# Optimization experiments

Measured on AMD Instinct MI355X. Metric: run time of the kernel, lower is better.

Reference implementation:

```python
import jax, jax.numpy as jnp
import numpy as np

N = 50000
E = 1600000

def setup_inputs() -> dict:
    key = jax.random.key(0)
    ks = jax.random.split(key, 8)
    x = jax.random.normal(ks[0], (N, 512), dtype=jnp.float32)
    edge_index = jax.random.randint(ks[1], (2, E), 0, N, dtype=jnp.int32).astype(jnp.int64)
    eigenvectors = jax.random.normal(ks[2], (N, 128), dtype=jnp.float32)
    W1 = jax.random.normal(ks[3], (512, 128), dtype=jnp.float32) * 0.04
    b1 = jnp.zeros((128,), dtype=jnp.float32)
    W2 = jax.random.normal(ks[4], (128, 64), dtype=jnp.float32) * 0.09
    b2 = jnp.zeros((64,), dtype=jnp.float32)
    lin_W = jax.random.normal(ks[5], (128, 64), dtype=jnp.float32) * 0.09
    W3 = jax.random.normal(ks[6], (128, 40), dtype=jnp.float32) * 0.09
    b3 = jnp.zeros((40,), dtype=jnp.float32)
    return {"x": x, "edge_index": edge_index, "eigenvectors": eigenvectors,
            "W1": W1, "b1": b1, "W2": W2, "b2": b2, "lin_W": lin_W, "W3": W3, "b3": b3}

def _gcn_norm(edge_index, num_nodes):
    # add self loops, then symmetric normalization D^-1/2 (A+I) D^-1/2
    loop = jnp.arange(num_nodes, dtype=edge_index.dtype)
    row = jnp.concatenate([edge_index[0], loop])  # source
    col = jnp.concatenate([edge_index[1], loop])  # target
    w = jnp.ones(row.shape[0], dtype=jnp.float32)
    deg = jax.ops.segment_sum(w, col, num_segments=num_nodes)
    dis = jnp.where(deg > 0, 1.0 / jnp.sqrt(deg), 0.0)
    norm = dis[row] * dis[col]  # [E+N]
    return row, col, norm

def _gcn_conv(h, W, b, row, col, norm, num_nodes):
    h = h @ W                                  # [N, d_out] linear first (PyG order)
    msg = h[row] * norm[:, None]               # gather + scale, [E+N, d_out]
    out = jax.ops.segment_sum(msg, col, num_segments=num_nodes)  # scatter-add
    return out + b

def reference(x, edge_index, eigenvectors, W1, b1, W2, b2, lin_W, W3, b3):
    num_nodes = x.shape[0]
    row, col, norm = _gcn_norm(edge_index, num_nodes)
    h = jax.nn.relu(_gcn_conv(x, W1, b1, row, col, norm, num_nodes))
    # dropout omitted: eval mode (deterministic reference)
    h = jax.nn.relu(_gcn_conv(h, W2, b2, row, col, norm, num_nodes))
    xp = eigenvectors @ lin_W                  # Linear(spec_in, spec_out, bias=False)
    h = jnp.concatenate([h, xp], axis=1)       # [N, h2+spec_out]
    h = _gcn_conv(h, W3, b3, row, col, norm, num_nodes)
    return jax.nn.log_softmax(h, axis=1)
```

## Files before the change

### kernel.cpp

```cpp
#include <hip/hip_runtime.h>
#include <cstdint>
#include <cstddef>

constexpr int BLK = 256;
constexpr int NB = 128;

static inline size_t ws_align(size_t x) { return (x + 255) & ~size_t(255); }

typedef __attribute__((ext_vector_type(8))) short bf16x8;
typedef __attribute__((ext_vector_type(4))) float f32x4;

__device__ inline unsigned short f2bf(float f) {
  unsigned int u = __float_as_uint(f);
  unsigned int r = (u + 0x7fffu + ((u >> 16) & 1u)) >> 16;
  return (unsigned short)r;
}
__device__ inline float bf2f(unsigned short u) {
  return __uint_as_float(((unsigned int)u) << 16);
}
__device__ inline float bf2f_lo(unsigned int w) {
  return __uint_as_float(w << 16);
}
__device__ inline float bf2f_hi(unsigned int w) {
  return __uint_as_float(w & 0xffff0000u);
}

__device__ inline void gload16(const void* gp, void* lp) {
  __builtin_amdgcn_global_load_lds(
      (const __attribute__((address_space(1))) void*)gp,
      (__attribute__((address_space(3))) void*)lp, 16, 0, 0);
}

__global__ void k_pack_wt(const int* __restrict__ ei, unsigned int* __restrict__ pk,
                          int* __restrict__ cnt, int E, int nChunk,
                          const float* __restrict__ W1, const float* __restrict__ W2,
                          const float* __restrict__ linW, const float* __restrict__ W3,
                          unsigned short* __restrict__ WT1, unsigned short* __restrict__ WT2,
                          unsigned short* __restrict__ WTl, unsigned short* __restrict__ WT3) {
  if (blockIdx.x >= NB) {
    int i = (blockIdx.x - NB) * BLK + threadIdx.x;
    if (i < 65536) {
      int n = i >> 9, k = i & 511;
      WT1[i] = f2bf(W1[(size_t)k * 128 + n]);
    } else if (i < 73728) {
      int j = i - 65536; int n = j >> 7, k = j & 127;
      WT2[j] = f2bf(W2[(size_t)k * 64 + n]);
    } else if (i < 81920) {
      int j = i - 73728; int n = j >> 7, k = j & 127;
      WTl[j] = f2bf(linW[(size_t)k * 64 + n]);
    } else if (i < 88064) {
      int j = i - 81920; int n = j >> 7, k = j & 127;
      WT3[j] = f2bf(n < 40 ? W3[(size_t)k * 40 + n] : 0.f);
    }
    return;
  }
  __shared__ int hist[256];
  for (int t = threadIdx.x; t < 256; t += BLK) hist[t] = 0;
  __syncthreads();
  int allz = 1;
  #pragma unroll 8
  for (int i = 0; i < 32; ++i) allz &= (ei[2 * i + 1] == 0) ? 1 : 0;
  const bool i64 = allz != 0;
  int beg = blockIdx.x * nChunk, end = min(beg + nChunk, E);
  for (int i = beg + threadIdx.x; i < end; i += BLK) {
    int row, col;
    if (i64) { row = ei[2 * i]; col = ei[2 * (E + i)]; }
    else     { row = ei[i];     col = ei[E + i]; }
    unsigned int p = ((unsigned int)col << 16) | (unsigned int)row;
    pk[i] = p;
    atomicAdd(&hist[col >> 8], 1);
  }
  __syncthreads();
  for (int t = threadIdx.x; t < 256; t += BLK) cnt[blockIdx.x * 256 + t] = hist[t];
}

__global__ void k_wscan(const int* __restrict__ cnt, int* __restrict__ woffs,
                        int* __restrict__ base, int nb, int E) {
  __shared__ int wsums[5];
  int w = threadIdx.x;
  int s = 0;
  for (int b = 0; b < nb; ++b) s += cnt[b * 256 + w];
  int lane = w & 63, wv = w >> 6;
  int x = s;
  #pragma unroll
  for (int sh = 1; sh < 64; sh <<= 1) { int t = __shfl_up(x, sh); if (lane >= sh) x += t; }
  if (lane == 63) wsums[wv] = x;
  __syncthreads();
  if (w == 0) { int a = 0; for (int k = 0; k < 4; ++k) { int t = wsums[k]; wsums[k] = a; a += t; } }
  __syncthreads();
  int excl = x - s + wsums[wv];
  woffs[w] = excl;
  if (w == 255) woffs[256] = excl + s;
  int start = excl;
  for (int b = 0; b < nb; ++b) { base[b * 256 + w] = start; start += cnt[b * 256 + w]; }
}

__global__ __launch_bounds__(256)
void k_part_gemm1(const unsigned int* __restrict__ pk, const int* __restrict__ base,
                  unsigned int* __restrict__ P, int E, int nChunk,
                  const float* __restrict__ x, const unsigned short* __restrict__ WT,
                  unsigned short* __restrict__ C, int N) {
  __shared__ __align__(16) char smem[49152];
  if (blockIdx.x < NB) {
    int* cur = (int*)smem;
    for (int t = threadIdx.x; t < 256; t += BLK) cur[t] = base[blockIdx.x * 256 + t];
    __syncthreads();
    int beg = blockIdx.x * nChunk, end = min(beg + nChunk, E);
    for (int i = beg + threadIdx.x; i < end; i += BLK) {
      unsigned int p = pk[i];
      int pos = atomicAdd(&cur[p >> 24], 1);
      P[pos] = p;
    }
    return;
  }
  float* As0 = (float*)smem;
  unsigned short* Wsl0 = (unsigned short*)(smem + 32768);
  const int tid = threadIdx.x;
  const int lane = tid & 63, wv = tid >> 6;
  const int m = lane & 15, kq = lane >> 4;
  const int row0 = ((int)blockIdx.x - NB) * 128;

  const int r8 = lane >> 3;
  const int c8 = lane & 7;
  int agrow[4];
  #pragma unroll
  for (int jj = 0; jj < 4; ++jj) {
    int gr = row0 + wv * 32 + jj * 8 + r8;
    agrow[jj] = gr < N ? gr : N - 1;
  }

  f32x4 acc[2][8];
  #pragma unroll
  for (int mr = 0; mr < 2; ++mr)
    #pragma unroll
    for (int t = 0; t < 8; ++t) acc[mr][t] = {0.f, 0.f, 0.f, 0.f};

  auto STAGE = [&](int pb, int kb) {
    #pragma unroll
    for (int jj = 0; jj < 4; ++jj) {
      const float* src = x + (size_t)agrow[jj] * 512 + kb * 32 + (c8 ^ r8) * 4;
      gload16(src, As0 + pb * 4096 + (wv * 32 + jj * 8) * 32);
    }
    #pragma unroll
    for (int jj = 0; jj < 2; ++jj) {
      int issue = wv * 2 + jj;
      int slot = issue >> 1, half = issue & 1;
      const unsigned short* src = WT + (size_t)(half * 64 + lane) * 512 + kb * 32 + slot * 8;
      gload16(src, Wsl0 + pb * 4096 + slot * 1024 + half * 512);
    }
  };

  STAGE(0, 0);
  __syncthreads();

  #pragma unroll 1
  for (int t = 0; t < 16; ++t) {
    const int p = t & 1;
    if (t < 15) STAGE(p ^ 1, t + 1);

    const char* Ab = (const char*)(As0 + p * 4096);
    const char* Wb = (const char*)(Wsl0 + p * 4096);
    bf16x8 af[2];
    #pragma unroll
    for (int mr = 0; mr < 2; ++mr) {
      int row = wv * 32 + mr * 16 + m;
      int s = row & 7;
      f32x4 lo = *(const f32x4*)(Ab + row * 128 + ((kq * 2) ^ s) * 16);
      f32x4 hi = *(const f32x4*)(Ab + row * 128 + ((kq * 2 + 1) ^ s) * 16);
      af[mr][0] = (short)f2bf(lo[0]); af[mr][1] = (short)f2bf(lo[1]);
      af[mr][2] = (short)f2bf(lo[2]); af[mr][3] = (short)f2bf(lo[3]);
      af[mr][4] = (short)f2bf(hi[0]); af[mr][5] = (short)f2bf(hi[1]);
      af[mr][6] = (short)f2bf(hi[2]); af[mr][7] = (short)f2bf(hi[3]);
    }
    #pragma unroll
    for (int tt = 0; tt < 8; ++tt) {
      bf16x8 bf = *(const bf16x8*)(Wb + kq * 2048 + (tt * 16 + m) * 16);
      #pragma unroll
      for (int mr = 0; mr < 2; ++mr)
        acc[mr][tt] = __builtin_amdgcn_mfma_f32_16x16x32_bf16(af[mr], bf, acc[mr][tt], 0, 0, 0);
    }
    __syncthreads();
  }

  #pragma unroll
  for (int mr = 0; mr < 2; ++mr)
    #pragma unroll
    for (int r = 0; r < 4; ++r) {
      int rr = row0 + wv * 32 + mr * 16 + kq * 4 + r;
      if (rr < N) {
        #pragma unroll
        for (int t = 0; t < 8; ++t)
          C[(size_t)rr * 128 + t * 16 + m] = f2bf(acc[mr][t][r]);
      }
    }
}

__global__ void k_window_build(const unsigned int* __restrict__ P,
                               const int* __restrict__ woffs,
                               float* __restrict__ dis, int* __restrict__ offs,
                               int* __restrict__ csr, int N, int E) {
  __shared__ int hist[256];
  __shared__ int wsums[5];
  __shared__ int lbase[256];
  const int node0 = blockIdx.x * 256;
  const int t = threadIdx.x;
  hist[t] = 0;
  __syncthreads();
  const int beg = woffs[blockIdx.x], end = woffs[blockIdx.x + 1];
  for (int i = beg + t; i < end; i += BLK)
    atomicAdd(&hist[(P[i] >> 16) & 255], 1);
  __syncthreads();
  const int dg = hist[t];
  if (node0 + t < N) dis[node0 + t] = 1.0f / sqrtf((float)(dg + 1));
  int lane = t & 63, wv = t >> 6;
  int x = dg;
  #pragma unroll
  for (int sh = 1; sh < 64; sh <<= 1) { int q = __shfl_up(x, sh); if (lane >= sh) x += q; }
  if (lane == 63) wsums[wv] = x;
  __syncthreads();
  if (t == 0) { int a = 0; for (int k = 0; k < 4; ++k) { int q = wsums[k]; wsums[k] = a; a += q; } }
  __syncthreads();
  const int goff = beg + (x - dg + wsums[wv]);
  if (node0 + t < N) offs[node0 + t] = goff;
  lbase[t] = goff;
  __syncthreads();
  for (int i = beg + t; i < end; i += BLK) {
    unsigned int p = P[i];
    int pos = atomicAdd(&lbase[(p >> 16) & 255], 1);
    csr[pos] = (int)(p & 0xffffu);
  }
  if (blockIdx.x == 0 && t == 0) offs[N] = E;
}

template<int NT, int MR, bool AF32>
__device__ inline void mgemm_body(int bi, const void* __restrict__ Av,
                                  const unsigned short* __restrict__ WT,
                                  const float* __restrict__ dis, unsigned short* __restrict__ C,
                                  int ldc, int NOUT, int N) {
  constexpr int K = 128;
  const int tid = threadIdx.x;
  const int lane = tid & 63;
  const int wv = tid >> 6;
  const int m = lane & 15;
  const int kq = lane >> 4;
  const int orow = bi * (64 * MR) + wv * (16 * MR);

  int rowc[MR];
  #pragma unroll
  for (int mr = 0; mr < MR; ++mr) {
    int row = orow + mr * 16 + m;
    rowc[mr] = row < N ? row : N - 1;
  }

  f32x4 acc[MR][NT];
  #pragma unroll
  for (int mr = 0; mr < MR; ++mr)
    #pragma unroll
    for (int t = 0; t < NT; ++t) acc[mr][t] = {0.f, 0.f, 0.f, 0.f};

  #pragma unroll 4
  for (int k0 = 0; k0 < K; k0 += 32) {
    bf16x8 af[MR];
    #pragma unroll
    for (int mr = 0; mr < MR; ++mr) {
      if constexpr (AF32) {
        const float* Arow = (const float*)Av + (size_t)rowc[mr] * K + kq * 8 + k0;
        float4 a0 = *(const float4*)Arow;
        float4 a1 = *(const float4*)(Arow + 4);
        af[mr][0] = (short)f2bf(a0.x); af[mr][1] = (short)f2bf(a0.y);
        af[mr][2] = (short)f2bf(a0.z); af[mr][3] = (short)f2bf(a0.w);
        af[mr][4] = (short)f2bf(a1.x); af[mr][5] = (short)f2bf(a1.y);
        af[mr][6] = (short)f2bf(a1.z); af[mr][7] = (short)f2bf(a1.w);
      } else {
        const unsigned short* Arow = (const unsigned short*)Av + (size_t)rowc[mr] * K + kq * 8 + k0;
        af[mr] = *(const bf16x8*)Arow;
      }
    }
    bf16x8 bf[NT];
    #pragma unroll
    for (int t = 0; t < NT; ++t)
      bf[t] = *(const bf16x8*)(WT + (size_t)(t * 16 + m) * K + k0 + kq * 8);
    #pragma unroll
    for (int t = 0; t < NT; ++t)
      #pragma unroll
      for (int mr = 0; mr < MR; ++mr)
        acc[mr][t] = __builtin_amdgcn_mfma_f32_16x16x32_bf16(af[mr], bf[t], acc[mr][t], 0, 0, 0);
  }
  #pragma unroll
  for (int mr = 0; mr < MR; ++mr) {
    #pragma unroll
    for (int r = 0; r < 4; ++r) {
      int rr = orow + mr * 16 + kq * 4 + r;
      if (rr < N) {
        float s = dis ? dis[rr] : 1.f;
        #pragma unroll
        for (int t = 0; t < NT; ++t) {
          int cc = t * 16 + m;
          if (cc < NOUT)
            C[(size_t)rr * ldc + cc] = f2bf(acc[mr][t][r] * s);
        }
      }
    }
  }
}

__global__ __launch_bounds__(256)
void k_mgemm2x(const unsigned short* __restrict__ G, const unsigned short* __restrict__ WT2,
               const float* __restrict__ dis, unsigned short* __restrict__ F,
               const float* __restrict__ eig, const unsigned short* __restrict__ WTl,
               unsigned short* __restrict__ XP, int N, int nA) {
  if ((int)blockIdx.x < nA)
    mgemm_body<4, 2, false>(blockIdx.x, G, WT2, dis, F, 64, 64, N);
  else
    mgemm_body<4, 2, true>(blockIdx.x - nA, eig, WTl, nullptr, XP, 64, 64, N);
}

__global__ __launch_bounds__(256)
void k_mgemm3(const unsigned short* __restrict__ H2, const unsigned short* __restrict__ XP,
              const unsigned short* __restrict__ WT3, const float* __restrict__ dis,
              unsigned short* __restrict__ C, int N) {
  constexpr int NT = 3, MR = 2;
  const int tid = threadIdx.x;
  const int lane = tid & 63;
  const int wv = tid >> 6;
  const int m = lane & 15;
  const int kq = lane >> 4;
  const int orow = blockIdx.x * (64 * MR) + wv * (16 * MR);

  int rowc[MR];
  #pragma unroll
  for (int mr = 0; mr < MR; ++mr) {
    int row = orow + mr * 16 + m;
    rowc[mr] = row < N ? row : N - 1;
  }

  f32x4 acc[MR][NT];
  #pragma unroll
  for (int mr = 0; mr < MR; ++mr)
    #pragma unroll
    for (int t = 0; t < NT; ++t) acc[mr][t] = {0.f, 0.f, 0.f, 0.f};

  #pragma unroll 4
  for (int k0 = 0; k0 < 128; k0 += 32) {
    const unsigned short* Abase = (k0 < 64) ? H2 : XP;
    const int kk = (k0 & 63) + kq * 8;
    bf16x8 af[MR];
    #pragma unroll
    for (int mr = 0; mr < MR; ++mr)
      af[mr] = *(const bf16x8*)(Abase + (size_t)rowc[mr] * 64 + kk);
    bf16x8 bf[NT];
    #pragma unroll
    for (int t = 0; t < NT; ++t)
      bf[t] = *(const bf16x8*)(WT3 + (size_t)(t * 16 + m) * 128 + k0 + kq * 8);
    #pragma unroll
    for (int t = 0; t < NT; ++t)
      #pragma unroll
      for (int mr = 0; mr < MR; ++mr)
        acc[mr][t] = __builtin_amdgcn_mfma_f32_16x16x32_bf16(af[mr], bf[t], acc[mr][t], 0, 0, 0);
  }
  #pragma unroll
  for (int mr = 0; mr < MR; ++mr) {
    #pragma unroll
    for (int r = 0; r < 4; ++r) {
      int rr = orow + mr * 16 + kq * 4 + r;
      if (rr < N) {
        float s = dis[rr];
        #pragma unroll
        for (int t = 0; t < NT; ++t) {
          int cc = t * 16 + m;
          if (cc < 40)
            C[(size_t)rr * 40 + cc] = f2bf(acc[mr][t][r] * s);
        }
      }
    }
  }
}

template<int D, bool RELU, bool GDIS>
__launch_bounds__(BLK)
__global__ void k_agg2(const unsigned short* __restrict__ g, int ldg,
                       const float* __restrict__ dis, const float* __restrict__ bias,
                       const int* __restrict__ offs, const int* __restrict__ csr,
                       unsigned short* __restrict__ dst, int ldd, int N) {
  constexpr int CPL = D / 32;
  int wid = (blockIdx.x * BLK + threadIdx.x) >> 6;
  int lane = threadIdx.x & 63;
  if (wid >= N) return;
  const int l5 = lane >> 5, c = lane & 31;
  const float dv = dis[wid];
  float acc[CPL];
  #pragma unroll
  for (int k = 0; k < CPL; ++k) acc[k] = 0.f;

  auto addrow = [&](int r, float w) {
    if constexpr (CPL == 4) {
      uint2 v = *(const uint2*)&g[(size_t)r * ldg + c * 4];
      acc[0] = fmaf(w, bf2f_lo(v.x), acc[0]); acc[1] = fmaf(w, bf2f_hi(v.x), acc[1]);
      acc[2] = fmaf(w, bf2f_lo(v.y), acc[2]); acc[3] = fmaf(w, bf2f_hi(v.y), acc[3]);
    } else {
      unsigned int v = *(const unsigned int*)&g[(size_t)r * ldg + c * 2];
      acc[0] = fmaf(w, bf2f_lo(v), acc[0]); acc[1] = fmaf(w, bf2f_hi(v), acc[1]);
    }
  };

  if (l5 == 0) addrow(wid, GDIS ? dv : 1.0f);
  int beg = offs[wid], end = offs[wid + 1];
  for (int e0 = beg; e0 < end; e0 += 64) {
    int cnt = end - e0; if (cnt > 64) cnt = 64;
    int u = (lane < cnt) ? csr[e0 + lane] : 0;
    float du = 1.0f;
    if constexpr (GDIS) du = (lane < cnt) ? dis[u] : 0.f;
    int j = 0;
    for (; j + 3 < cnt; j += 4) {
      int r0 = __shfl(u, j + l5);
      int r1 = __shfl(u, j + 2 + l5);
      float w0 = GDIS ? __shfl(du, j + l5) : 1.0f;
      float w1 = GDIS ? __shfl(du, j + 2 + l5) : 1.0f;
      addrow(r0, w0); addrow(r1, w1);
    }
    for (; j < cnt; j += 2) {
      int jj = j + l5;
      int si = jj < cnt ? jj : j;
      int r0 = __shfl(u, si);
      float w0 = GDIS ? __shfl(du, si) : 1.0f;
      if (jj < cnt) addrow(r0, w0);
    }
  }
  #pragma unroll
  for (int k = 0; k < CPL; ++k) acc[k] += __shfl_xor(acc[k], 32);

  if (l5 == 0) {
    float o[CPL];
    #pragma unroll
    for (int k = 0; k < CPL; ++k) {
      o[k] = dv * acc[k] + bias[c * CPL + k];
      if constexpr (RELU) o[k] = fmaxf(o[k], 0.f);
    }
    if constexpr (CPL == 4) {
      uint2 pw;
      pw.x = (unsigned)f2bf(o[0]) | ((unsigned)f2bf(o[1]) << 16);
      pw.y = (unsigned)f2bf(o[2]) | ((unsigned)f2bf(o[3]) << 16);
      *(uint2*)&dst[(size_t)wid * ldd + c * 4] = pw;
    } else {
      unsigned int pw = (unsigned)f2bf(o[0]) | ((unsigned)f2bf(o[1]) << 16);
      *(unsigned int*)&dst[(size_t)wid * ldd + c * 2] = pw;
    }
  }
}

__launch_bounds__(BLK)
__global__ void k_agg40(const unsigned short* __restrict__ g,
                        const float* __restrict__ dis, const float* __restrict__ bias,
                        const int* __restrict__ offs, const int* __restrict__ csr,
                        float* __restrict__ dst, int N) {
  int wid = (blockIdx.x * BLK + threadIdx.x) >> 6;
  int lane = threadIdx.x & 63;
  if (wid >= N) return;
  const int l5 = lane >> 5, c = lane & 31;
  const bool act = c < 20;
  float a0 = 0.f, a1 = 0.f;
  auto addrow = [&](int r) {
    if (act) {
      unsigned int w = *(const unsigned int*)&g[(size_t)r * 40 + c * 2];
      a0 += bf2f_lo(w); a1 += bf2f_hi(w);
    }
  };
  if (l5 == 0) addrow(wid);
  int beg = offs[wid], end = offs[wid + 1];
  for (int e0 = beg; e0 < end; e0 += 64) {
    int cnt = end - e0; if (cnt > 64) cnt = 64;
    int u = (lane < cnt) ? csr[e0 + lane] : 0;
    int j = 0;
    for (; j + 3 < cnt; j += 4) {
      int r0 = __shfl(u, j + l5);
      int r1 = __shfl(u, j + 2 + l5);
      addrow(r0); addrow(r1);
    }
    for (; j < cnt; j += 2) {
      int jj = j + l5;
      int r0 = __shfl(u, jj < cnt ? jj : j);
      if (jj < cnt) addrow(r0);
    }
  }
  a0 += __shfl_xor(a0, 32);
  a1 += __shfl_xor(a1, 32);

  if (l5 == 0) {
    float dv = dis[wid];
    float o0 = act ? dv * a0 + bias[c * 2]     : -__builtin_inff();
    float o1 = act ? dv * a1 + bias[c * 2 + 1] : -__builtin_inff();
    float mx = fmaxf(o0, o1);
    #pragma unroll
    for (int s = 16; s >= 1; s >>= 1) mx = fmaxf(mx, __shfl_down(mx, s, 32));
    mx = __shfl(mx, 0, 32);
    float ex = act ? (expf(o0 - mx) + expf(o1 - mx)) : 0.f;
    #pragma unroll
    for (int s = 16; s >= 1; s >>= 1) ex += __shfl_down(ex, s, 32);
    float ls = logf(__shfl(ex, 0, 32));
    if (act) {
      float2 r = make_float2(o0 - mx - ls, o1 - mx - ls);
      *(float2*)&dst[(size_t)wid * 40 + c * 2] = r;
    }
  }
}

extern "C" void kernel_launch(void* const* d_in, const int* in_sizes, int n_in,
                              void* d_out, int out_size, void* d_ws, size_t ws_size,
                              hipStream_t stream) {
  const float* x    = (const float*)d_in[0];
  const int*   ei   = (const int*)d_in[1];
  const float* eig  = (const float*)d_in[2];
  const float* W1   = (const float*)d_in[3];
  const float* b1   = (const float*)d_in[4];
  const float* W2   = (const float*)d_in[5];
  const float* b2   = (const float*)d_in[6];
  const float* linW = (const float*)d_in[7];
  const float* W3   = (const float*)d_in[8];
  const float* b3   = (const float*)d_in[9];
  float* out = (float*)d_out;

  const int N = in_sizes[0] / 512;
  const int E = in_sizes[1] / 2;

  char* ws = (char*)d_ws;
  size_t off = 0;
  auto alloc = [&](size_t bytes) { char* p = ws + off; off = ws_align(off + bytes); return p; };
  unsigned int* pk = (unsigned int*)alloc((size_t)E * 4);
  unsigned int* P  = (unsigned int*)alloc((size_t)E * 4);
  int*   csr    = (int*)alloc((size_t)E * 4);
  int*   offs   = (int*)alloc((size_t)(N + 1) * 4);
  int*   cnt    = (int*)alloc((size_t)NB * 256 * 4);
  int*   base   = (int*)alloc((size_t)NB * 256 * 4);
  int*   woffs  = (int*)alloc(257 * 4);
  float* dis    = (float*)alloc((size_t)N * 4);
  unsigned short* F  = (unsigned short*)alloc((size_t)N * 128 * 2);
  unsigned short* G  = (unsigned short*)alloc((size_t)N * 128 * 2);
  unsigned short* XP = (unsigned short*)alloc((size_t)N * 64 * 2);
  unsigned short* H2 = (unsigned short*)alloc((size_t)N * 64 * 2);
  unsigned short* WT1 = (unsigned short*)alloc(128 * 512 * 2);
  unsigned short* WT2 = (unsigned short*)alloc(64 * 128 * 2);
  unsigned short* WTl = (unsigned short*)alloc(64 * 128 * 2);
  unsigned short* WT3 = (unsigned short*)alloc(48 * 128 * 2);

  const int nChunk = (E + NB - 1) / NB;
  const int NW = (N + 255) / 256;
  const int WTB = (88064 + BLK - 1) / BLK;
  const int gG1 = (N + 127) / 128;
  const int gA = (N + 3) / 4;

  k_pack_wt<<<NB + WTB, BLK, 0, stream>>>(ei, pk, cnt, E, nChunk,
                                          W1, W2, linW, W3, WT1, WT2, WTl, WT3);
  k_wscan<<<1, 256, 0, stream>>>(cnt, woffs, base, NB, E);
  k_part_gemm1<<<NB + gG1, BLK, 0, stream>>>(pk, base, P, E, nChunk, x, WT1, F, N);
  k_window_build<<<NW, BLK, 0, stream>>>(P, woffs, dis, offs, csr, N, E);

  k_agg2<128, true, true><<<gA, BLK, 0, stream>>>(F, 128, dis, b1, offs, csr, G, 128, N);
  k_mgemm2x<<<2 * gG1, BLK, 0, stream>>>(G, WT2, dis, F, eig, WTl, XP, N, gG1);
  k_agg2<64, true, false><<<gA, BLK, 0, stream>>>(F, 64, dis, b2, offs, csr, H2, 64, N);
  k_mgemm3<<<gG1, BLK, 0, stream>>>(H2, XP, WT3, dis, F, N);
  k_agg40<<<gA, BLK, 0, stream>>>(F, dis, b3, offs, csr, out, N);
}
```

Measured before the change: 286.0 us.

## Triple-buffer GEMM1 staging with one barrier per step and reorder block roles

The GEMM part of the fused partition/GEMM1 kernel moves from double to triple LDS buffering. Each iteration now waits on the vector-memory counter for the previous stage only and uses a single raw barrier instead of two __syncthreads, so the next tile's loads overlap more of the MFMA work. GEMM blocks now take the low block indices and the edge-partition blocks come last, which changes dispatch order. Shared memory grows from 48KB to 72KB per block, which may reduce how many blocks fit on each CU.

```diff
diff --git a/kernel.cpp b/kernel.cpp
--- a/kernel.cpp
+++ b/kernel.cpp
@@ -99,13 +99,14 @@
 void k_part_gemm1(const unsigned int* __restrict__ pk, const int* __restrict__ base,
                   unsigned int* __restrict__ P, int E, int nChunk,
                   const float* __restrict__ x, const unsigned short* __restrict__ WT,
-                  unsigned short* __restrict__ C, int N) {
-  __shared__ __align__(16) char smem[49152];
-  if (blockIdx.x < NB) {
+                  unsigned short* __restrict__ C, int N, int gG1) {
+  __shared__ __align__(16) char smem[73728];
+  if ((int)blockIdx.x >= gG1) {
+    const int pb = (int)blockIdx.x - gG1;
     int* cur = (int*)smem;
-    for (int t = threadIdx.x; t < 256; t += BLK) cur[t] = base[blockIdx.x * 256 + t];
+    for (int t = threadIdx.x; t < 256; t += BLK) cur[t] = base[pb * 256 + t];
     __syncthreads();
-    int beg = blockIdx.x * nChunk, end = min(beg + nChunk, E);
+    int beg = pb * nChunk, end = min(beg + nChunk, E);
     for (int i = beg + threadIdx.x; i < end; i += BLK) {
       unsigned int p = pk[i];
       int pos = atomicAdd(&cur[p >> 24], 1);
@@ -114,11 +115,11 @@
     return;
   }
   float* As0 = (float*)smem;
-  unsigned short* Wsl0 = (unsigned short*)(smem + 32768);
+  unsigned short* Wsl0 = (unsigned short*)(smem + 49152);
   const int tid = threadIdx.x;
   const int lane = tid & 63, wv = tid >> 6;
   const int m = lane & 15, kq = lane >> 4;
-  const int row0 = ((int)blockIdx.x - NB) * 128;
+  const int row0 = (int)blockIdx.x * 128;
 
   const int r8 = lane >> 3;
   const int c8 = lane & 7;
@@ -151,15 +152,21 @@
   };
 
   STAGE(0, 0);
-  __syncthreads();
-
+  int cur = 0;
   #pragma unroll 1
   for (int t = 0; t < 16; ++t) {
-    const int p = t & 1;
-    if (t < 15) STAGE(p ^ 1, t + 1);
-
-    const char* Ab = (const char*)(As0 + p * 4096);
-    const char* Wb = (const char*)(Wsl0 + p * 4096);
+    int nxt = cur + 1; if (nxt == 3) nxt = 0;
+    if (t < 15) {
+      STAGE(nxt, t + 1);
+      asm volatile("s_waitcnt vmcnt(6)" ::: "memory");
+    } else {
+      asm volatile("s_waitcnt vmcnt(0)" ::: "memory");
+    }
+    __builtin_amdgcn_s_barrier();
+    __builtin_amdgcn_sched_barrier(0);
+
+    const char* Ab = (const char*)(As0 + cur * 4096);
+    const char* Wb = (const char*)(Wsl0 + cur * 4096);
     bf16x8 af[2];
     #pragma unroll
     for (int mr = 0; mr < 2; ++mr) {
@@ -179,7 +186,7 @@
       for (int mr = 0; mr < 2; ++mr)
         acc[mr][tt] = __builtin_amdgcn_mfma_f32_16x16x32_bf16(af[mr], bf, acc[mr][tt], 0, 0, 0);
     }
-    __syncthreads();
+    cur = nxt;
   }
 
   #pragma unroll
@@ -551,7 +558,7 @@
   k_pack_wt<<<NB + WTB, BLK, 0, stream>>>(ei, pk, cnt, E, nChunk,
                                           W1, W2, linW, W3, WT1, WT2, WTl, WT3);
   k_wscan<<<1, 256, 0, stream>>>(cnt, woffs, base, NB, E);
-  k_part_gemm1<<<NB + gG1, BLK, 0, stream>>>(pk, base, P, E, nChunk, x, WT1, F, N);
+  k_part_gemm1<<<gG1 + NB, BLK, 0, stream>>>(pk, base, P, E, nChunk, x, WT1, F, N, gG1);
   k_window_build<<<NW, BLK, 0, stream>>>(P, woffs, dis, offs, csr, N, E);
 
   k_agg2<128, true, true><<<gA, BLK, 0, stream>>>(F, 128, dis, b1, offs, csr, G, 128, N);
```

New measurement: 289.1 us. No clear change (+1.1%).
